# Performance work log

Hardware: AMD Instinct MI355X
Metric: run time of the kernel (lower is better)

Reference implementation:

```python
import math
import jax, jax.numpy as jnp
import numpy as np

N_HEAD = 16
LORA_SCALE = 16.0 / 8.0  # lora_alpha / r


def lora_linear(x, W, b, A, B):
    # y = x @ W^T + b + scale * (x @ A^T) @ B^T
    base = jnp.einsum('btc,oc->bto', x, W) + b
    low = jnp.einsum('btc,rc->btr', x, A)
    return base + LORA_SCALE * jnp.einsum('btr,or->bto', low, B)


def setup_inputs() -> dict:
    key = jax.random.key(0)
    ks = jax.random.split(key, 8)
    B, T, C = 2, 2048, 1024
    r = 8
    s = 0.02
    return {
        'x': jax.random.normal(ks[0], (B, T, C), jnp.float32),
        'W_attn': jax.random.normal(ks[1], (3 * C, C), jnp.float32) * s,
        'b_attn': jnp.zeros((3 * C,), jnp.float32),
        'A_attn': jax.random.normal(ks[2], (r, C), jnp.float32) * s,
        'B_attn': jax.random.normal(ks[3], (3 * C, r), jnp.float32) * s,
        'W_proj': jax.random.normal(ks[4], (C, C), jnp.float32) * s,
        'b_proj': jnp.zeros((C,), jnp.float32),
        'A_proj': jax.random.normal(ks[5], (r, C), jnp.float32) * s,
        'B_proj': jax.random.normal(ks[6], (C, r), jnp.float32) * s,
    }


def reference(x, W_attn, b_attn, A_attn, B_attn, W_proj, b_proj, A_proj, B_proj):
    B, T, C = x.shape
    H = N_HEAD
    hd = C // H
    qkv = lora_linear(x, W_attn, b_attn, A_attn, B_attn)  # [B,T,3C]
    q, k, v = jnp.split(qkv, 3, axis=2)
    # [B,H,T,hd]
    q = q.reshape(B, T, H, hd).transpose(0, 2, 1, 3)
    k = k.reshape(B, T, H, hd).transpose(0, 2, 1, 3)
    v = v.reshape(B, T, H, hd).transpose(0, 2, 1, 3)
    att = jnp.einsum('bhqd,bhkd->bhqk', q, k) * (1.0 / math.sqrt(hd))
    causal = jnp.tril(jnp.ones((T, T), bool))
    att = jnp.where(causal, att, -jnp.inf)
    att = jax.nn.softmax(att, axis=-1)
    out = jnp.einsum('bhqk,bhkd->bhqd', att, v)
    out = out.transpose(0, 2, 1, 3).reshape(B, T, C)
    return lora_linear(out, W_proj, b_proj, A_proj, B_proj)
```

## Files before the change

kernel.cpp:

```cpp
#include <hip/hip_runtime.h>
#include <hip/hip_bf16.h>
#include <stdint.h>

typedef __bf16 bf16_t;
typedef __bf16 bf16x8 __attribute__((ext_vector_type(8)));
typedef __bf16 bf16x4 __attribute__((ext_vector_type(4)));
typedef __bf16 bf16x2 __attribute__((ext_vector_type(2)));
typedef float f32x4 __attribute__((ext_vector_type(4)));
typedef float f32x16 __attribute__((ext_vector_type(16)));
typedef uint32_t u32;
typedef uint32_t u32x4 __attribute__((ext_vector_type(4)));

typedef __attribute__((address_space(1))) void as1void;
typedef __attribute__((address_space(3))) void as3void;

#define QSCALE 0.18033688011112042f

__constant__ unsigned char kOrder[24] = {7, 22, 23, 20, 21, 6, 18, 19, 16, 17,
                                         5, 14, 15, 12, 13, 4, 10, 11, 8, 9,
                                         3, 2, 1, 0};

__device__ __forceinline__ void gll16(const void* g, void* l) {
  __builtin_amdgcn_global_load_lds((as1void*)g, (as3void*)l, 16, 0, 0);
}

__device__ __forceinline__ u32 pack2(float a, float b) {
  bf16x2 t = {(bf16_t)a, (bf16_t)b};
  return __builtin_bit_cast(u32, t);
}

__global__ void prep_all(const float* __restrict__ W_attn, const float* __restrict__ B_attn,
                         const float* __restrict__ A_attn, const float* __restrict__ W_proj,
                         const float* __restrict__ B_proj, const float* __restrict__ A_proj,
                         const float4* __restrict__ x,
                         bf16_t* __restrict__ WaE, bf16_t* __restrict__ WpE,
                         bf16x4* __restrict__ Xb) {
  int bid = blockIdx.x;
  if (bid < 16384) {
    int idx = bid * 256 + threadIdx.x;
    const float *W, *Bm, *Am;
    bf16_t* dst;
    if (idx < 3145728) {
      W = W_attn; Bm = B_attn; Am = A_attn; dst = WaE;
    } else {
      idx -= 3145728;
      W = W_proj; Bm = B_proj; Am = A_proj; dst = WpE;
    }
    int o = idx >> 10, c = idx & 1023;
    float acc = W[idx];
#pragma unroll
    for (int r = 0; r < 8; ++r)
      acc += 2.0f * Bm[o * 8 + r] * Am[r * 1024 + c];
    dst[idx] = (bf16_t)acc;
  } else {
    int i = (bid - 16384) * 256 + threadIdx.x;
    float4 v = x[i];
    bf16x4 o = {(bf16_t)v.x, (bf16_t)v.y, (bf16_t)v.z, (bf16_t)v.w};
    Xb[i] = o;
  }
}

__global__ __launch_bounds__(256) void transpose_v(
    const bf16_t* __restrict__ Vb, bf16_t* __restrict__ Vtg) {
  __shared__ bf16_t Lt[128][72];
  int blk = blockIdx.x;
  int bh = blk >> 4, tb = blk & 15;
  int t0 = tb * 128;
  int tid = threadIdx.x;
  {
    int t = tid >> 1, dc = (tid & 1) * 32;
    const bf16_t* p = Vb + (size_t)bh * 131072 + (size_t)(t0 + t) * 64 + dc;
#pragma unroll
    for (int u = 0; u < 4; ++u)
      *(bf16x8*)&Lt[t][dc + u * 8] = *(const bf16x8*)(p + u * 8);
  }
  __syncthreads();
  int d = tid & 63, tg = tid >> 6;
  bf16_t* q = Vtg + (size_t)bh * 131072 + (size_t)d * 2048 + t0 + tg * 32;
#pragma unroll
  for (int u = 0; u < 4; ++u) {
    bf16x8 v;
#pragma unroll
    for (int e = 0; e < 8; ++e) v[e] = Lt[tg * 32 + u * 8 + e][d];
    *(bf16x8*)(q + u * 8) = v;
  }
}

template <bool QKV>
__global__ __launch_bounds__(256, 3) void gemm_bt(
    const bf16_t* __restrict__ A, const bf16_t* __restrict__ Bt,
    const float* __restrict__ bias,
    bf16_t* __restrict__ Qb, bf16_t* __restrict__ Kb, bf16_t* __restrict__ Vb,
    float* __restrict__ Out) {
  __shared__ bf16_t Als[128][64];
  __shared__ bf16_t Bls[128][64];
  const int m0 = blockIdx.x * 128;
  const int n0 = blockIdx.y * 128;
  const int tid = threadIdx.x;
  const int lane = tid & 63;
  const int w = tid >> 6;
  const int wm = w >> 1, wn = w & 1;
  const int lr = lane & 15, g = lane >> 4;
  const int sw = (lane & 7) << 3;
  const int srow = lane >> 3;
  const int soff = ((lane & 7) ^ srow) * 8;

  f32x4 acc[4][4] = {};

  for (int k0 = 0; k0 < 1024; k0 += 64) {
#pragma unroll
    for (int c = 0; c < 4; ++c) {
      int r = w * 32 + c * 8 + srow;
      gll16(A + (size_t)(m0 + r) * 1024 + k0 + soff, &Als[w * 32 + c * 8][0]);
      gll16(Bt + (size_t)(n0 + r) * 1024 + k0 + soff, &Bls[w * 32 + c * 8][0]);
    }
    __syncthreads();
#pragma unroll
    for (int ks = 0; ks < 2; ++ks) {
      bf16x8 af[4], bfv[4];
#pragma unroll
      for (int i = 0; i < 4; ++i)
        af[i] = *(const bf16x8*)&Als[wm * 64 + i * 16 + lr][(ks * 32 + g * 8) ^ sw];
#pragma unroll
      for (int j = 0; j < 4; ++j)
        bfv[j] = *(const bf16x8*)&Bls[wn * 64 + j * 16 + lr][(ks * 32 + g * 8) ^ sw];
#pragma unroll
      for (int i = 0; i < 4; ++i)
#pragma unroll
        for (int j = 0; j < 4; ++j)
          acc[i][j] = __builtin_amdgcn_mfma_f32_16x16x32_bf16(af[i], bfv[j], acc[i][j], 0, 0, 0);
    }
    __syncthreads();
  }

#pragma unroll
  for (int i = 0; i < 4; ++i) {
#pragma unroll
    for (int j = 0; j < 4; ++j) {
#pragma unroll
      for (int e = 0; e < 4; ++e) {
        int m = m0 + wm * 64 + i * 16 + g * 4 + e;
        int n = n0 + wn * 64 + j * 16 + lr;
        float v = acc[i][j][e] + bias[n];
        if (QKV) {
          int b = m >> 11, t = m & 2047;
          int which = n >> 10, hn = n & 1023;
          int h = hn >> 6, d = hn & 63;
          if (which == 0) v *= QSCALE;
          bf16_t* dst = (which == 0) ? Qb : (which == 1) ? Kb : Vb;
          dst[(((size_t)(b * 16 + h)) * 2048 + t) * 64 + d] = (bf16_t)v;
        } else {
          Out[(size_t)m * 1024 + n] = v;
        }
      }
    }
  }
}

__global__ __launch_bounds__(256, 3) void attn_fwd(
    const bf16_t* __restrict__ Qb, const bf16_t* __restrict__ Kb,
    const bf16_t* __restrict__ Vtg, bf16_t* __restrict__ Ob,
    bf16_t* __restrict__ Po, float* __restrict__ Pml) {
  __shared__ bf16_t Kls[3][64][64];
  __shared__ bf16_t Vt[3][64][64];

  int id = blockIdx.x;
  int xcd = id & 7, r = id >> 3;
  int bh = xcd * 4 + (r & 3);
  int j = kOrder[r >> 2];
  int qb, kt0, kt1, part;
  if (j < 8) {
    qb = j; kt0 = 0; kt1 = 2 * qb + 2; part = -1;
  } else {
    qb = 8 + ((j - 8) >> 1);
    part = (j - 8) & 1;
    int nA = qb + 1;
    kt0 = part ? nA : 0;
    kt1 = part ? (2 * qb + 2) : nA;
  }
  int b = bh >> 4, h = bh & 15;

  const int tid = threadIdx.x, lane = tid & 63, w = tid >> 6;
  const int q32 = lane & 31;
  const int hi = lane >> 5;
  const int ksw = (q32 & 7) << 3;
  const bf16_t* Qp = Qb + (size_t)bh * 2048 * 64;
  const bf16_t* Kp = Kb + (size_t)bh * 2048 * 64;
  const bf16_t* Vtp = Vtg + (size_t)bh * 131072;

  const int q0 = qb * 128;
  const int qrow = q0 + w * 32 + q32;

  const int sr = lane >> 3;
  const int sc = ((lane & 7) ^ sr) * 8;
  int vdo[2];
#pragma unroll
  for (int c = 0; c < 2; ++c)
    vdo[c] = (w * 16 + c * 8 + sr) * 2048 + sc;

  bf16x8 qf[4];
#pragma unroll
  for (int ds = 0; ds < 4; ++ds)
    qf[ds] = *(const bf16x8*)(Qp + (size_t)qrow * 64 + ds * 16 + hi * 8);

  float m_run = -3e38f, l_run = 0.f;
  f32x16 o_acc[2] = {};

  {
    const int kp = kt0 * 64;
#pragma unroll
    for (int c = 0; c < 2; ++c) {
      int rb = w * 16 + c * 8;
      gll16(Kp + (size_t)(kp + rb + sr) * 64 + sc, &Kls[0][rb][0]);
      gll16(Vtp + vdo[c] + kp, &Vt[0][rb][0]);
    }
    const int kp1 = kp + 64;
#pragma unroll
    for (int c = 0; c < 2; ++c) {
      int rb = w * 16 + c * 8;
      gll16(Kp + (size_t)(kp1 + rb + sr) * 64 + sc, &Kls[1][rb][0]);
      gll16(Vtp + vdo[c] + kp1, &Vt[1][rb][0]);
    }
    asm volatile("s_waitcnt vmcnt(4)" ::: "memory");
    __builtin_amdgcn_s_barrier();
  }

  int cb = 0;
  for (int kt = kt0; kt < kt1; ++kt) {
    const bool pf2 = (kt + 2 < kt1);
    const int pf = (cb >= 1) ? cb - 1 : 2;

    if (pf2) {
      const int kn = (kt + 2) * 64;
#pragma unroll
      for (int c = 0; c < 2; ++c) {
        int rb = w * 16 + c * 8;
        gll16(Kp + (size_t)(kn + rb + sr) * 64 + sc, &Kls[pf][rb][0]);
        gll16(Vtp + vdo[c] + kn, &Vt[pf][rb][0]);
      }
    }

    const int rel = kt - 2 * qb;
    int nfa = 2, dfa = -1;
    if (rel == 0) {
      if (w == 0) { nfa = 1; dfa = 0; }
      else if (w == 1) { dfa = 1; }
    } else if (rel == 1) {
      if (w < 2) nfa = 0;
      else if (w == 2) { nfa = 1; dfa = 0; }
      else { dfa = 1; }
    }

    if (nfa > 0) {
      f32x16 s[2] = {};
      __builtin_amdgcn_s_setprio(1);
#pragma unroll
      for (int fa = 0; fa < 2; ++fa) {
        if (fa < nfa) {
#pragma unroll
          for (int ds = 0; ds < 4; ++ds) {
            bf16x8 kf = *(const bf16x8*)&Kls[cb][fa * 32 + q32][(ds * 16 + hi * 8) ^ ksw];
            s[fa] = __builtin_amdgcn_mfma_f32_32x32x16_bf16(kf, qf[ds], s[fa], 0, 0, 0);
          }
        }
      }
      __builtin_amdgcn_s_setprio(0);

      float mloc = -3e38f;
#pragma unroll
      for (int fa = 0; fa < 2; ++fa) {
        if (fa < nfa) {
          if (fa == dfa) {
#pragma unroll
            for (int rr = 0; rr < 16; ++rr) {
              int km = (rr & 3) + 8 * (rr >> 2) + 4 * hi;
              if (km > q32) s[fa][rr] = -3e38f;
            }
          }
#pragma unroll
          for (int rr = 0; rr < 16; rr += 2)
            mloc = fmaxf(mloc, fmaxf(s[fa][rr], s[fa][rr + 1]));
        }
      }
      mloc = fmaxf(mloc, __shfl_xor(mloc, 32, 64));
      if (!__all(mloc <= m_run + 8.0f)) {
        float mnew = fmaxf(m_run, mloc);
        float rs = __builtin_amdgcn_exp2f(m_run - mnew);
        m_run = mnew;
        l_run *= rs;
        o_acc[0] *= rs;
        o_acc[1] *= rs;
      }

      float lsum = 0.f;
#pragma unroll
      for (int fa = 0; fa < 2; ++fa) {
        if (fa < nfa) {
          float p[16];
#pragma unroll
          for (int rr = 0; rr < 16; ++rr) {
            p[rr] = __builtin_amdgcn_exp2f(s[fa][rr] - m_run);
            lsum += p[rr];
          }
          u32 x0 = pack2(p[0], p[1]),   x1 = pack2(p[2], p[3]);
          u32 x2 = pack2(p[4], p[5]),   x3 = pack2(p[6], p[7]);
          u32 y0 = pack2(p[8], p[9]),   y1 = pack2(p[10], p[11]);
          u32 y2 = pack2(p[12], p[13]), y3 = pack2(p[14], p[15]);
          u32 z0 = hi ? x0 : x2;
          u32 z1 = hi ? x1 : x3;
          u32 z2 = hi ? y0 : y2;
          u32 z3 = hi ? y1 : y3;
          z0 = (u32)__shfl_xor((int)z0, 32, 64);
          z1 = (u32)__shfl_xor((int)z1, 32, 64);
          z2 = (u32)__shfl_xor((int)z2, 32, 64);
          z3 = (u32)__shfl_xor((int)z3, 32, 64);
          u32x4 pw0 = hi ? (u32x4){z0, z1, x2, x3} : (u32x4){x0, x1, z0, z1};
          u32x4 pw1 = hi ? (u32x4){z2, z3, y2, y3} : (u32x4){y0, y1, z2, z3};
          bf16x8 P0 = __builtin_bit_cast(bf16x8, pw0);
          bf16x8 P1 = __builtin_bit_cast(bf16x8, pw1);
          __builtin_amdgcn_s_setprio(1);
#pragma unroll
          for (int db = 0; db < 2; ++db) {
            int d = db * 32 + q32;
            bf16x8 vf0 = *(const bf16x8*)&Vt[cb][d][(fa * 32 + hi * 8) ^ ksw];
            o_acc[db] = __builtin_amdgcn_mfma_f32_32x32x16_bf16(vf0, P0, o_acc[db], 0, 0, 0);
            bf16x8 vf1 = *(const bf16x8*)&Vt[cb][d][(fa * 32 + 16 + hi * 8) ^ ksw];
            o_acc[db] = __builtin_amdgcn_mfma_f32_32x32x16_bf16(vf1, P1, o_acc[db], 0, 0, 0);
          }
          __builtin_amdgcn_s_setprio(0);
        }
      }
      lsum += __shfl_xor(lsum, 32, 64);
      l_run += lsum;
    }

    if (pf2) {
      asm volatile("s_waitcnt vmcnt(4)" ::: "memory");
    } else {
      asm volatile("s_waitcnt vmcnt(0)" ::: "memory");
    }
    __builtin_amdgcn_s_barrier();
    cb = (cb == 2) ? 0 : cb + 1;
  }

  const int prow = w * 32 + q32;
  if (part < 0) {
    float inv = 1.0f / l_run;
    bf16_t* obase = Ob + ((size_t)(b * 2048 + qrow)) * 1024 + h * 64;
#pragma unroll
    for (int db = 0; db < 2; ++db) {
#pragma unroll
      for (int rg = 0; rg < 4; ++rg) {
        bf16x4 ov = {(bf16_t)(o_acc[db][rg * 4 + 0] * inv),
                     (bf16_t)(o_acc[db][rg * 4 + 1] * inv),
                     (bf16_t)(o_acc[db][rg * 4 + 2] * inv),
                     (bf16_t)(o_acc[db][rg * 4 + 3] * inv)};
        *(bf16x4*)(obase + db * 32 + rg * 8 + hi * 4) = ov;
      }
    }
  } else {
    int sidx = bh * 16 + (qb - 8) * 2 + part;
    bf16_t* po = (part == 0)
        ? Ob + ((size_t)(b * 2048 + qrow)) * 1024 + h * 64
        : Po + (size_t)(bh * 8 + (qb - 8)) * 8192 + prow * 64;
#pragma unroll
    for (int db = 0; db < 2; ++db) {
#pragma unroll
      for (int rg = 0; rg < 4; ++rg) {
        bf16x4 ov = {(bf16_t)o_acc[db][rg * 4 + 0], (bf16_t)o_acc[db][rg * 4 + 1],
                     (bf16_t)o_acc[db][rg * 4 + 2], (bf16_t)o_acc[db][rg * 4 + 3]};
        *(bf16x4*)(po + db * 32 + rg * 8 + hi * 4) = ov;
      }
    }
    if (hi == 0) {
      Pml[sidx * 256 + prow * 2] = m_run;
      Pml[sidx * 256 + prow * 2 + 1] = l_run;
    }
  }
}

__global__ __launch_bounds__(256) void attn_merge(
    const bf16_t* __restrict__ Po, const float* __restrict__ Pml,
    bf16_t* __restrict__ Ob) {
  int blk = blockIdx.x;
  int bh = blk >> 3, qb8 = blk & 7;
  int qb = 8 + qb8;
  int b = bh >> 4, h = bh & 15;
  int sA = bh * 16 + qb8 * 2, sB = sA + 1;
  int t = threadIdx.x;
  int row = t >> 1, c0 = (t & 1) * 32;

  float mA = Pml[sA * 256 + row * 2], lA = Pml[sA * 256 + row * 2 + 1];
  float mB = Pml[sB * 256 + row * 2], lB = Pml[sB * 256 + row * 2 + 1];
  float m = fmaxf(mA, mB);
  float wA = __builtin_amdgcn_exp2f(mA - m);
  float wB = __builtin_amdgcn_exp2f(mB - m);
  float inv = 1.0f / (lA * wA + lB * wB);
  wA *= inv;
  wB *= inv;

  bf16_t* ob = Ob + ((size_t)(b * 2048 + qb * 128 + row)) * 1024 + h * 64 + c0;
  const bf16_t* pb = Po + (size_t)(bh * 8 + qb8) * 8192 + row * 64 + c0;
#pragma unroll
  for (int u = 0; u < 4; ++u) {
    bf16x8 a = *(const bf16x8*)(ob + u * 8);
    bf16x8 c = *(const bf16x8*)(pb + u * 8);
    bf16x8 o;
#pragma unroll
    for (int i = 0; i < 8; ++i)
      o[i] = (bf16_t)((float)a[i] * wA + (float)c[i] * wB);
    *(bf16x8*)(ob + u * 8) = o;
  }
}

extern "C" void kernel_launch(void* const* d_in, const int* in_sizes, int n_in,
                              void* d_out, int out_size, void* d_ws, size_t ws_size,
                              hipStream_t stream) {
  const float* x      = (const float*)d_in[0];
  const float* W_attn = (const float*)d_in[1];
  const float* b_attn = (const float*)d_in[2];
  const float* A_attn = (const float*)d_in[3];
  const float* B_attn = (const float*)d_in[4];
  const float* W_proj = (const float*)d_in[5];
  const float* b_proj = (const float*)d_in[6];
  const float* A_proj = (const float*)d_in[7];
  const float* B_proj = (const float*)d_in[8];
  float* out = (float*)d_out;

  char* ws = (char*)d_ws;
  bf16_t* WaE = (bf16_t*)(ws);
  bf16_t* WpE = (bf16_t*)(ws + 6291456);
  bf16_t* Xb  = (bf16_t*)(ws + 8388608);
  bf16_t* Qb  = (bf16_t*)(ws + 16777216);
  bf16_t* Kb  = (bf16_t*)(ws + 25165824);
  bf16_t* Vb  = (bf16_t*)(ws + 33554432);
  bf16_t* Ob  = (bf16_t*)(ws + 41943040);
  bf16_t* Vtg = (bf16_t*)(ws + 8388608);
  bf16_t* Po  = (bf16_t*)(ws);
  float*  Pml = (float*)(ws + 4194304);

  prep_all<<<20480, 256, 0, stream>>>(W_attn, B_attn, A_attn, W_proj, B_proj, A_proj,
                                      (const float4*)x, WaE, WpE, (bf16x4*)Xb);

  gemm_bt<true><<<dim3(32, 24), 256, 0, stream>>>(Xb, WaE, b_attn, Qb, Kb, Vb, nullptr);
  transpose_v<<<512, 256, 0, stream>>>(Vb, Vtg);
  attn_fwd<<<768, 256, 0, stream>>>(Qb, Kb, Vtg, Ob, Po, Pml);
  attn_merge<<<256, 256, 0, stream>>>(Po, Pml, Ob);
  gemm_bt<false><<<dim3(32, 8), 256, 0, stream>>>(Ob, WpE, b_proj, nullptr, nullptr, nullptr, out);
}
```

Baseline: 115.1 us.

## Use larger double-buffered 256x192 tiles with 512 threads for QKV GEMM

The templated GEMM is split into a dedicated QKV kernel and a projection kernel. The QKV kernel uses 512-thread blocks with 256x192 tiles, giving 256 blocks instead of 768, which should roughly fill the CUs in one wave. It double-buffers LDS with async global-to-LDS loads so the next K tile is prefetched while MFMAs run on the current one. The goal is more operand reuse per load and less load latency exposed, at the cost of higher LDS use per block, which may lower occupancy.

```diff
diff --git a/kernel.cpp b/kernel.cpp
--- a/kernel.cpp
+++ b/kernel.cpp
@@ -86,12 +86,89 @@
   }
 }
 
-template <bool QKV>
-__global__ __launch_bounds__(256, 3) void gemm_bt(
+__global__ __launch_bounds__(512, 2) void gemm_qkv(
     const bf16_t* __restrict__ A, const bf16_t* __restrict__ Bt,
     const float* __restrict__ bias,
-    bf16_t* __restrict__ Qb, bf16_t* __restrict__ Kb, bf16_t* __restrict__ Vb,
-    float* __restrict__ Out) {
+    bf16_t* __restrict__ Qb, bf16_t* __restrict__ Kb, bf16_t* __restrict__ Vb) {
+  __shared__ bf16_t Als[2][256][64];
+  __shared__ bf16_t Bls[2][192][64];
+  const int m0 = blockIdx.x * 256;
+  const int n0 = blockIdx.y * 192;
+  const int tid = threadIdx.x;
+  const int lane = tid & 63;
+  const int w = tid >> 6;
+  const int wr = w >> 2;
+  const int wc = w & 3;
+  const int lr = lane & 15, g = lane >> 4;
+  const int sw = (lane & 7) << 3;
+  const int srow = lane >> 3;
+  const int soff = ((lane & 7) ^ srow) * 8;
+
+  f32x4 acc[8][3] = {};
+
+#pragma unroll
+  for (int c = 0; c < 4; ++c)
+    gll16(A + (size_t)(m0 + w * 32 + c * 8 + srow) * 1024 + soff,
+          &Als[0][w * 32 + c * 8][0]);
+#pragma unroll
+  for (int c = 0; c < 3; ++c)
+    gll16(Bt + (size_t)(n0 + w * 24 + c * 8 + srow) * 1024 + soff,
+          &Bls[0][w * 24 + c * 8][0]);
+  __syncthreads();
+
+  for (int kt = 0; kt < 16; ++kt) {
+    const int cbuf = kt & 1, nbuf = cbuf ^ 1;
+    if (kt + 1 < 16) {
+      const int k1 = (kt + 1) * 64;
+#pragma unroll
+      for (int c = 0; c < 4; ++c)
+        gll16(A + (size_t)(m0 + w * 32 + c * 8 + srow) * 1024 + k1 + soff,
+              &Als[nbuf][w * 32 + c * 8][0]);
+#pragma unroll
+      for (int c = 0; c < 3; ++c)
+        gll16(Bt + (size_t)(n0 + w * 24 + c * 8 + srow) * 1024 + k1 + soff,
+              &Bls[nbuf][w * 24 + c * 8][0]);
+    }
+#pragma unroll
+    for (int ks = 0; ks < 2; ++ks) {
+      bf16x8 bfv[3];
+#pragma unroll
+      for (int j = 0; j < 3; ++j)
+        bfv[j] = *(const bf16x8*)&Bls[cbuf][wc * 48 + j * 16 + lr][(ks * 32 + g * 8) ^ sw];
+#pragma unroll
+      for (int i = 0; i < 8; ++i) {
+        bf16x8 af = *(const bf16x8*)&Als[cbuf][wr * 128 + i * 16 + lr][(ks * 32 + g * 8) ^ sw];
+#pragma unroll
+        for (int j = 0; j < 3; ++j)
+          acc[i][j] = __builtin_amdgcn_mfma_f32_16x16x32_bf16(af, bfv[j], acc[i][j], 0, 0, 0);
+      }
+    }
+    __syncthreads();
+  }
+
+#pragma unroll
+  for (int i = 0; i < 8; ++i) {
+#pragma unroll
+    for (int j = 0; j < 3; ++j) {
+#pragma unroll
+      for (int e = 0; e < 4; ++e) {
+        int m = m0 + wr * 128 + i * 16 + g * 4 + e;
+        int n = n0 + wc * 48 + j * 16 + lr;
+        float v = acc[i][j][e] + bias[n];
+        int b = m >> 11, t = m & 2047;
+        int which = n >> 10, hn = n & 1023;
+        int h = hn >> 6, d = hn & 63;
+        if (which == 0) v *= QSCALE;
+        bf16_t* dst = (which == 0) ? Qb : (which == 1) ? Kb : Vb;
+        dst[(((size_t)(b * 16 + h)) * 2048 + t) * 64 + d] = (bf16_t)v;
+      }
+    }
+  }
+}
+
+__global__ __launch_bounds__(256, 3) void gemm_proj(
+    const bf16_t* __restrict__ A, const bf16_t* __restrict__ Bt,
+    const float* __restrict__ bias, float* __restrict__ Out) {
   __shared__ bf16_t Als[128][64];
   __shared__ bf16_t Bls[128][64];
   const int m0 = blockIdx.x * 128;
@@ -141,17 +218,7 @@
       for (int e = 0; e < 4; ++e) {
         int m = m0 + wm * 64 + i * 16 + g * 4 + e;
         int n = n0 + wn * 64 + j * 16 + lr;
-        float v = acc[i][j][e] + bias[n];
-        if (QKV) {
-          int b = m >> 11, t = m & 2047;
-          int which = n >> 10, hn = n & 1023;
-          int h = hn >> 6, d = hn & 63;
-          if (which == 0) v *= QSCALE;
-          bf16_t* dst = (which == 0) ? Qb : (which == 1) ? Kb : Vb;
-          dst[(((size_t)(b * 16 + h)) * 2048 + t) * 64 + d] = (bf16_t)v;
-        } else {
-          Out[(size_t)m * 1024 + n] = v;
-        }
+        Out[(size_t)m * 1024 + n] = acc[i][j][e] + bias[n];
       }
     }
   }
@@ -442,9 +509,9 @@
   prep_all<<<20480, 256, 0, stream>>>(W_attn, B_attn, A_attn, W_proj, B_proj, A_proj,
                                       (const float4*)x, WaE, WpE, (bf16x4*)Xb);
 
-  gemm_bt<true><<<dim3(32, 24), 256, 0, stream>>>(Xb, WaE, b_attn, Qb, Kb, Vb, nullptr);
+  gemm_qkv<<<dim3(16, 16), 512, 0, stream>>>(Xb, WaE, b_attn, Qb, Kb, Vb);
   transpose_v<<<512, 256, 0, stream>>>(Vb, Vtg);
   attn_fwd<<<768, 256, 0, stream>>>(Qb, Kb, Vtg, Ob, Po, Pml);
   attn_merge<<<256, 256, 0, stream>>>(Po, Pml, Ob);
-  gemm_bt<false><<<dim3(32, 8), 256, 0, stream>>>(Ob, WpE, b_proj, nullptr, nullptr, nullptr, out);
-}
+  gemm_proj<<<dim3(32, 8), 256, 0, stream>>>(Ob, WpE, b_proj, out);
+}
```

Result: no change. 114.2 us (-0.8%).

## Triple-buffer GEMM k-tiles with async LDS prefetch and single barrier per step

Applied to the files above, without the earlier changes.

Replaces the synchronous load-then-compute GEMM main loop (K-step 64, two barriers per step) with a three-stage ring of 32-wide K tiles. Global-to-LDS loads for tile k+2 are issued while tile k is being multiplied, with vmcnt waits and one barrier per iteration. It also raises wave priority around the MFMA block. The goal is to hide global load latency behind the matrix math, at the cost of twice as many loop iterations and a new XOR swizzle that has to match the read pattern.

```diff
diff --git a/kernel.cpp b/kernel.cpp
--- a/kernel.cpp
+++ b/kernel.cpp
@@ -87,13 +87,13 @@
 }
 
 template <bool QKV>
-__global__ __launch_bounds__(256, 3) void gemm_bt(
+__global__ __launch_bounds__(256, 3) void gemm_bt32(
     const bf16_t* __restrict__ A, const bf16_t* __restrict__ Bt,
     const float* __restrict__ bias,
     bf16_t* __restrict__ Qb, bf16_t* __restrict__ Kb, bf16_t* __restrict__ Vb,
     float* __restrict__ Out) {
-  __shared__ bf16_t Als[128][64];
-  __shared__ bf16_t Bls[128][64];
+  __shared__ bf16_t Als[3][128][32];
+  __shared__ bf16_t Bls[3][128][32];
   const int m0 = blockIdx.x * 128;
   const int n0 = blockIdx.y * 128;
   const int tid = threadIdx.x;
@@ -101,36 +101,63 @@
   const int w = tid >> 6;
   const int wm = w >> 1, wn = w & 1;
   const int lr = lane & 15, g = lane >> 4;
-  const int sw = (lane & 7) << 3;
-  const int srow = lane >> 3;
-  const int soff = ((lane & 7) ^ srow) * 8;
+  const int kcol = ((g ^ (lr & 3)) * 8);
+  const int sr = lane >> 2;
+  const int ssrc = (((lane & 3) ^ (sr & 3)) * 8);
 
   f32x4 acc[4][4] = {};
 
-  for (int k0 = 0; k0 < 1024; k0 += 64) {
-#pragma unroll
-    for (int c = 0; c < 4; ++c) {
-      int r = w * 32 + c * 8 + srow;
-      gll16(A + (size_t)(m0 + r) * 1024 + k0 + soff, &Als[w * 32 + c * 8][0]);
-      gll16(Bt + (size_t)(n0 + r) * 1024 + k0 + soff, &Bls[w * 32 + c * 8][0]);
-    }
-    __syncthreads();
-#pragma unroll
-    for (int ks = 0; ks < 2; ++ks) {
-      bf16x8 af[4], bfv[4];
-#pragma unroll
-      for (int i = 0; i < 4; ++i)
-        af[i] = *(const bf16x8*)&Als[wm * 64 + i * 16 + lr][(ks * 32 + g * 8) ^ sw];
+#pragma unroll
+  for (int c = 0; c < 2; ++c) {
+    int rb = w * 32 + c * 16;
+    gll16(A + (size_t)(m0 + rb + sr) * 1024 + ssrc, &Als[0][rb][0]);
+    gll16(Bt + (size_t)(n0 + rb + sr) * 1024 + ssrc, &Bls[0][rb][0]);
+  }
+#pragma unroll
+  for (int c = 0; c < 2; ++c) {
+    int rb = w * 32 + c * 16;
+    gll16(A + (size_t)(m0 + rb + sr) * 1024 + 32 + ssrc, &Als[1][rb][0]);
+    gll16(Bt + (size_t)(n0 + rb + sr) * 1024 + 32 + ssrc, &Bls[1][rb][0]);
+  }
+  asm volatile("s_waitcnt vmcnt(4)" ::: "memory");
+  __builtin_amdgcn_s_barrier();
+
+  int cb = 0;
+  for (int kt = 0; kt < 32; ++kt) {
+    const bool pf2 = (kt + 2 < 32);
+    const int pf = (cb >= 1) ? cb - 1 : 2;
+    if (pf2) {
+      const int kn = (kt + 2) * 32;
+#pragma unroll
+      for (int c = 0; c < 2; ++c) {
+        int rb = w * 32 + c * 16;
+        gll16(A + (size_t)(m0 + rb + sr) * 1024 + kn + ssrc, &Als[pf][rb][0]);
+        gll16(Bt + (size_t)(n0 + rb + sr) * 1024 + kn + ssrc, &Bls[pf][rb][0]);
+      }
+    }
+
+    bf16x8 af[4], bfv[4];
+#pragma unroll
+    for (int i = 0; i < 4; ++i)
+      af[i] = *(const bf16x8*)&Als[cb][wm * 64 + i * 16 + lr][kcol];
+#pragma unroll
+    for (int j = 0; j < 4; ++j)
+      bfv[j] = *(const bf16x8*)&Bls[cb][wn * 64 + j * 16 + lr][kcol];
+    __builtin_amdgcn_s_setprio(1);
+#pragma unroll
+    for (int i = 0; i < 4; ++i)
 #pragma unroll
       for (int j = 0; j < 4; ++j)
-        bfv[j] = *(const bf16x8*)&Bls[wn * 64 + j * 16 + lr][(ks * 32 + g * 8) ^ sw];
-#pragma unroll
-      for (int i = 0; i < 4; ++i)
-#pragma unroll
-        for (int j = 0; j < 4; ++j)
-          acc[i][j] = __builtin_amdgcn_mfma_f32_16x16x32_bf16(af[i], bfv[j], acc[i][j], 0, 0, 0);
-    }
-    __syncthreads();
+        acc[i][j] = __builtin_amdgcn_mfma_f32_16x16x32_bf16(af[i], bfv[j], acc[i][j], 0, 0, 0);
+    __builtin_amdgcn_s_setprio(0);
+
+    if (pf2) {
+      asm volatile("s_waitcnt vmcnt(4)" ::: "memory");
+    } else {
+      asm volatile("s_waitcnt vmcnt(0)" ::: "memory");
+    }
+    __builtin_amdgcn_s_barrier();
+    cb = (cb == 2) ? 0 : cb + 1;
   }
 
 #pragma unroll
@@ -442,9 +469,9 @@
   prep_all<<<20480, 256, 0, stream>>>(W_attn, B_attn, A_attn, W_proj, B_proj, A_proj,
                                       (const float4*)x, WaE, WpE, (bf16x4*)Xb);
 
-  gemm_bt<true><<<dim3(32, 24), 256, 0, stream>>>(Xb, WaE, b_attn, Qb, Kb, Vb, nullptr);
+  gemm_bt32<true><<<dim3(32, 24), 256, 0, stream>>>(Xb, WaE, b_attn, Qb, Kb, Vb, nullptr);
   transpose_v<<<512, 256, 0, stream>>>(Vb, Vtg);
   attn_fwd<<<768, 256, 0, stream>>>(Qb, Kb, Vtg, Ob, Po, Pml);
   attn_merge<<<256, 256, 0, stream>>>(Po, Pml, Ob);
-  gemm_bt<false><<<dim3(32, 8), 256, 0, stream>>>(Ob, WpE, b_proj, nullptr, nullptr, nullptr, out);
-}
+  gemm_bt32<false><<<dim3(32, 8), 256, 0, stream>>>(Ob, WpE, b_proj, nullptr, nullptr, nullptr, out);
+}
```

After: 120.6 us. +4.7%, slower.
